# Performance work log

Measured on AMD Instinct MI355X. Metric: run time of the kernel, lower is better.

## Reference

```python
import jax, jax.numpy as jnp
import numpy as np

NUM_HEADS = 32
HEAD_DIM = 128
ROPE_THETA = 10000.0


def _rope_tables(seq_len, head_dim, theta):
    inv_freq = 1.0 / (theta ** (jnp.arange(0, head_dim, 2, dtype=jnp.float32) / head_dim))
    pos = jnp.arange(seq_len, dtype=jnp.float32)
    freqs = pos[:, None] * inv_freq[None, :]            # [S, hd/2]
    emb = jnp.concatenate([freqs, freqs], axis=-1)      # [S, hd]
    return jnp.cos(emb), jnp.sin(emb)


def _rotate_half(x):
    x1, x2 = jnp.split(x, 2, axis=-1)
    return jnp.concatenate([-x2, x1], axis=-1)


def _apply_rope(x, cos, sin):
    # x: [B, S, H, D]; cos/sin: [S, D] -> unsqueeze_dim=2 broadcasting
    c = cos[None, :, None, :]
    s = sin[None, :, None, :]
    return x * c + _rotate_half(x) * s


def setup_inputs() -> dict:
    key = jax.random.key(0)
    ks = jax.random.split(key, 6)
    hidden = 4096
    B, S = 2, 4096  # global sequence = world_size * local_seq (4 * 1024)
    hidden_states = jax.random.normal(ks[0], (B, S, hidden), dtype=jnp.float32)
    # original uses torch.rand (uniform); scaled by 0.02 for numerical sanity
    q_proj = jax.random.uniform(ks[1], (hidden, hidden), dtype=jnp.float32) * 0.02
    k_proj = jax.random.uniform(ks[2], (hidden, hidden), dtype=jnp.float32) * 0.02
    v_proj = jax.random.uniform(ks[3], (hidden, hidden), dtype=jnp.float32) * 0.02
    o_proj = jax.random.uniform(ks[4], (hidden, hidden), dtype=jnp.float32) * 0.02
    return {"hidden_states": hidden_states, "q_proj": q_proj, "k_proj": k_proj,
            "v_proj": v_proj, "o_proj": o_proj, "world_size": 4}


def _ring_attention(hidden_states, q_proj, k_proj, v_proj, o_proj, world_size):
    B, S, H = hidden_states.shape
    s_local = S // world_size
    nh, hd = NUM_HEADS, HEAD_DIM
    scale = 1.0 / np.sqrt(hd).astype(np.float32)

    # rank 0 holds the first sequence shard as its local hidden states
    hs_local = hidden_states[:, :s_local]
    q = (hs_local @ q_proj.T).reshape(B, s_local, nh, hd)
    k = (hidden_states @ k_proj.T).reshape(B, S, nh, hd)
    v = (hidden_states @ v_proj.T).reshape(B, S, nh, hd)

    cos, sin = _rope_tables(S, hd, ROPE_THETA)
    q = _apply_rope(q, cos[:s_local], sin[:s_local])   # rank0 positions 0..s_local-1
    k = _apply_rope(k, cos, sin)                       # global positions per shard

    # split into per-rank KV blocks; rank 0 receives blocks W-1, W-2, ..., 0
    k_blocks = k.reshape(B, world_size, s_local, nh, hd).transpose(1, 0, 2, 3, 4)[::-1]
    v_blocks = v.reshape(B, world_size, s_local, nh, hd).transpose(1, 0, 2, 3, 4)[::-1]

    def step(carry, kv):
        attn, max_lse, denom, lse_full = carry
        k_blk, v_blk = kv
        # memory_efficient_attention_partial: non-causal partial attention + lse
        s = jnp.einsum('bqhd,bkhd->bhqk', q, k_blk) * scale
        m = jnp.max(s, axis=-1)                          # [B,H,q]
        p = jnp.exp(s - m[..., None])
        l = jnp.sum(p, axis=-1)
        lse = (m + jnp.log(l)).transpose(0, 2, 1)        # [B,q,H]
        out = jnp.einsum('bhqk,bkhd->bqhd', p / l[..., None], v_blk)
        # online-softmax merge across ring steps
        new_max = jnp.maximum(max_lse, lse)
        old_adj = jnp.exp(max_lse - new_max)[..., None]
        new_adj = jnp.exp(lse - new_max)[..., None]
        denom = old_adj * denom + new_adj
        attn = old_adj * attn + new_adj * out
        lse_full = new_max + jnp.log(jnp.exp(lse_full - new_max) + jnp.exp(lse - new_max))
        return (attn, new_max, denom, lse_full), None

    init = (jnp.zeros((B, s_local, nh, hd), jnp.float32),
            jnp.full((B, s_local, nh), -jnp.inf, jnp.float32),
            jnp.zeros((B, s_local, nh, 1), jnp.float32),
            jnp.full((B, s_local, nh), -jnp.inf, jnp.float32))
    (attn, _, denom, _), _ = jax.lax.scan(step, init, (k_blocks, v_blocks))

    attn = attn / denom
    attn = attn.astype(jnp.float16).astype(jnp.float32)  # .half() in source
    attn = attn.reshape(B, s_local, nh * hd)
    return attn @ o_proj.T


def reference(hidden_states, q_proj, k_proj, v_proj, o_proj, world_size):
    return _ring_attention(hidden_states, q_proj, k_proj, v_proj, o_proj, world_size)
```

## Files before the change

kernel.cpp:

```cpp
#include <hip/hip_runtime.h>
#include <hip/hip_bf16.h>


using bf16x8 = __attribute__((ext_vector_type(8))) short;
using f32x4  = __attribute__((ext_vector_type(4))) float;

__device__ inline unsigned short f32_to_bf16_bits(float f) {
  unsigned int u = __float_as_uint(f);
  u += 0x7FFFu + ((u >> 16) & 1u);
  return (unsigned short)(u >> 16);
}
__device__ inline float bf16_bits_to_f32(unsigned short h) {
  return __uint_as_float(((unsigned int)h) << 16);
}
__device__ inline unsigned short f32_to_bf16_fast(float f) {
  __hip_bfloat16 hb = __float2bfloat16(f);
  unsigned short us;
  __builtin_memcpy(&us, &hb, 2);
  return us;
}

__device__ __forceinline__ void load_lds16(const unsigned short* g, unsigned short* l) {
  __builtin_amdgcn_global_load_lds(
      (const __attribute__((address_space(1))) void*)g,
      (__attribute__((address_space(3))) void*)l, 16, 0, 0);
}

__global__ void cast_f32_bf16_batched(const float* __restrict__ hs,
                                      const float* __restrict__ w0,
                                      const float* __restrict__ w1,
                                      const float* __restrict__ w2,
                                      const float* __restrict__ w3,
                                      unsigned short* __restrict__ out) {
  const long hs4 = 2L * 4096 * 4096 / 4;
  const long w4  = 4096L * 4096 / 4;
  long i = (long)blockIdx.x * blockDim.x + threadIdx.x;
  long stride = (long)gridDim.x * blockDim.x;
  const long total = hs4 + 4 * w4;
  for (; i < total; i += stride) {
    const float* src;
    long j = i;
    if (j < hs4) { src = hs; }
    else {
      j -= hs4;
      long wi = j / w4;
      j -= wi * w4;
      src = (wi == 0) ? w0 : (wi == 1) ? w1 : (wi == 2) ? w2 : w3;
    }
    float4 v = reinterpret_cast<const float4*>(src)[j];
    ushort4 o;
    o.x = f32_to_bf16_bits(v.x);
    o.y = f32_to_bf16_bits(v.y);
    o.z = f32_to_bf16_bits(v.z);
    o.w = f32_to_bf16_bits(v.w);
    reinterpret_cast<ushort4*>(out)[i] = o;
  }
}

__global__ void rope_tables(float* __restrict__ cos_t, float* __restrict__ sin_t) {
  int idx = blockIdx.x * 256 + threadIdx.x;
  if (idx >= 4096 * 64) return;
  int p = idx >> 6, i = idx & 63;
  float inv = __expf(-(float)i * (9.210340371976184f / 64.0f));
  float f = (float)p * inv;
  cos_t[idx] = cosf(f);
  sin_t[idx] = sinf(f);
}

__global__ void rope_apply_qk(unsigned short* __restrict__ qbuf,
                              unsigned short* __restrict__ kbuf,
                              const float4* __restrict__ cos4,
                              const float4* __restrict__ sin4,
                              float qgain) {
  const long qch = 2048L * 256;
  const long kch = 8192L * 256;
  long idx = (long)blockIdx.x * 256 + threadIdx.x;
  if (idx >= qch + kch) return;
  unsigned short* buf;
  int pos_mask; float gain;
  if (idx < qch) { buf = qbuf; pos_mask = 1023; gain = qgain; }
  else { idx -= qch; buf = kbuf; pos_mask = 4095; gain = 1.0f; }
  long tok = idx >> 8;
  int rem = (int)(idx & 255);
  int head = rem >> 3, c = rem & 7;
  int pos = (int)(tok & (long)pos_mask);
  float4 ct0 = cos4[pos * 16 + c * 2];
  float4 ct1 = cos4[pos * 16 + c * 2 + 1];
  float4 st0 = sin4[pos * 16 + c * 2];
  float4 st1 = sin4[pos * 16 + c * 2 + 1];
  float cs[8] = {ct0.x, ct0.y, ct0.z, ct0.w, ct1.x, ct1.y, ct1.z, ct1.w};
  float sn[8] = {st0.x, st0.y, st0.z, st0.w, st1.x, st1.y, st1.z, st1.w};
  long base = tok * 4096 + head * 128 + c * 8;
  bf16x8 x1 = *reinterpret_cast<const bf16x8*>(buf + base);
  bf16x8 x2 = *reinterpret_cast<const bf16x8*>(buf + base + 64);
  bf16x8 o1, o2;
#pragma unroll
  for (int j = 0; j < 8; j++) {
    float a = bf16_bits_to_f32((unsigned short)x1[j]);
    float b = bf16_bits_to_f32((unsigned short)x2[j]);
    o1[j] = (short)f32_to_bf16_bits((a * cs[j] - b * sn[j]) * gain);
    o2[j] = (short)f32_to_bf16_bits((b * cs[j] + a * sn[j]) * gain);
  }
  *reinterpret_cast<bf16x8*>(buf + base) = o1;
  *reinterpret_cast<bf16x8*>(buf + base + 64) = o2;
}

__device__ inline void storeC(float* p, float v) { *p = v; }
__device__ inline void storeC(unsigned short* p, float v) { *p = f32_to_bf16_bits(v); }

#define STG2(Gb, Lb, h, kc)                                                    \
  load_lds16((Gb) + (long)((h) * 128 + srow) * 4096 + sslot * 8 + (kc),        \
             (Lb) + tid * 8);                                                  \
  load_lds16((Gb) + (long)((h) * 128 + 64 + srow) * 4096 + sslot * 8 + (kc),   \
             (Lb) + 4096 + tid * 8);

#define MFMAQ(MH, NH)                                                          \
  _Pragma("unroll") for (int mi = 0; mi < 4; ++mi)                             \
    _Pragma("unroll") for (int ni = 0; ni < 2; ++ni)                           \
      _Pragma("unroll") for (int kk = 0; kk < 2; ++kk)                         \
        acc[(MH) * 4 + mi][(NH) * 2 + ni] =                                    \
            __builtin_amdgcn_mfma_f32_16x16x32_bf16(                           \
                a[mi][kk], b[(NH) * 2 + ni][kk],                               \
                acc[(MH) * 4 + mi][(NH) * 2 + ni], 0, 0, 0);

#define TILE(P, KC, MODE)                                                      \
  {                                                                            \
    const unsigned short* Ar = lds + wm * 16384 + (P) * 8192;                  \
    const unsigned short* Br =                                                 \
        lds + 32768 + (wn >> 1) * 16384 + (P) * 8192 + (wn & 1) * 4096;        \
    _Pragma("unroll") for (int mf = 0; mf < 4; ++mf) {                         \
      a[mf][0] = *reinterpret_cast<const bf16x8*>(Ar + mf * 1024 + ao0);       \
      a[mf][1] = *reinterpret_cast<const bf16x8*>(Ar + mf * 1024 + ao1);       \
    }                                                                          \
    _Pragma("unroll") for (int nf = 0; nf < 2; ++nf) {                         \
      b[nf][0] = *reinterpret_cast<const bf16x8*>(Br + nf * 1024 + ao0);       \
      b[nf][1] = *reinterpret_cast<const bf16x8*>(Br + nf * 1024 + ao1);       \
    }                                                                          \
    __builtin_amdgcn_s_setprio(1);                                             \
    MFMAQ(0, 0);                                                               \
    __builtin_amdgcn_s_setprio(0);                                             \
    _Pragma("unroll") for (int nf = 2; nf < 4; ++nf) {                         \
      b[nf][0] = *reinterpret_cast<const bf16x8*>(Br + nf * 1024 + ao0);       \
      b[nf][1] = *reinterpret_cast<const bf16x8*>(Br + nf * 1024 + ao1);       \
    }                                                                          \
    __builtin_amdgcn_s_setprio(1);                                             \
    MFMAQ(0, 1);                                                               \
    __builtin_amdgcn_s_setprio(0);                                             \
    asm volatile("s_waitcnt lgkmcnt(0)" ::: "memory");                         \
    asm volatile("s_barrier" ::: "memory");            \
    if ((MODE) == 0) {                                                         \
      STG2(Bg, lds + 32768 + (P) * 8192, 0, KC);                               \
      STG2(Bg, lds + 49152 + (P) * 8192, 1, KC);                               \
    }                                                                          \
    _Pragma("unroll") for (int mf = 0; mf < 4; ++mf) {                         \
      a[mf][0] = *reinterpret_cast<const bf16x8*>(Ar + (4 + mf) * 1024 + ao0); \
      a[mf][1] = *reinterpret_cast<const bf16x8*>(Ar + (4 + mf) * 1024 + ao1); \
    }                                                                          \
    __builtin_amdgcn_s_setprio(1);                                             \
    MFMAQ(1, 0);                                                               \
    __builtin_amdgcn_s_setprio(0);                                             \
    asm volatile("s_waitcnt lgkmcnt(0)" ::: "memory");                         \
    asm volatile("s_barrier" ::: "memory");            \
    if ((MODE) == 0) {                                                         \
      STG2(Ag, lds + (P) * 8192, 0, KC);                                       \
      STG2(Ag, lds + 16384 + (P) * 8192, 1, KC);                               \
    }                                                                          \
    __builtin_amdgcn_s_setprio(1);                                             \
    MFMAQ(1, 1);                                                               \
    __builtin_amdgcn_s_setprio(0);                                             \
    if ((MODE) == 0) asm volatile("s_waitcnt vmcnt(8)" ::: "memory");          \
    if ((MODE) == 1) asm volatile("s_waitcnt vmcnt(0)" ::: "memory");          \
    asm volatile("s_barrier" ::: "memory");       \
  }

template <typename OUT_T>
__global__ __launch_bounds__(512, 2) void gemm256(const unsigned short* __restrict__ A,
                                                  const unsigned short* __restrict__ B,
                                                  OUT_T* __restrict__ C,
                                                  long Astride_z, long Cstride_z, int N) {
  __shared__ unsigned short lds[65536];
  const int tid = threadIdx.x;
  const int bn = blockIdx.x, bm = blockIdx.y, bz = blockIdx.z;
  const unsigned short* Ag = A + (long)bz * Astride_z + (long)bm * 256 * 4096;
  const unsigned short* Bg = B + (long)bn * 256 * 4096;

  const int w = tid >> 6, lane = tid & 63;
  const int wm = w >> 2, wn = w & 3;
  const int fr = lane & 15, fg = lane >> 4;
  const int ao0 = fr * 64 + ((fg ^ (fr & 7)) * 8);
  const int ao1 = fr * 64 + (((4 + fg) ^ (fr & 7)) * 8);
  const int srow = tid >> 3;
  const int sslot = (tid & 7) ^ (srow & 7);

  f32x4 acc[8][4] = {};
  bf16x8 a[4][2], b[4][2];

  STG2(Ag, lds + 0, 0, 0);     STG2(Ag, lds + 16384, 1, 0);
  STG2(Bg, lds + 32768, 0, 0); STG2(Bg, lds + 49152, 1, 0);
  STG2(Ag, lds + 8192, 0, 64);  STG2(Ag, lds + 24576, 1, 64);
  STG2(Bg, lds + 40960, 0, 64); STG2(Bg, lds + 57344, 1, 64);
  asm volatile("s_waitcnt vmcnt(8)" ::: "memory");
  asm volatile("s_barrier" ::: "memory");

  for (int ti = 0; ti < 31; ++ti) {
    TILE(0, (2 * ti + 2) * 64, 0);
    TILE(1, (2 * ti + 3) * 64, 0);
  }
  TILE(0, 0, 1);
  TILE(1, 0, 2);

  OUT_T* Cb = C + (long)bz * Cstride_z + ((long)bm * 256) * N + bn * 256;
#pragma unroll
  for (int mf = 0; mf < 8; ++mf)
#pragma unroll
    for (int nf = 0; nf < 4; ++nf)
#pragma unroll
      for (int rr = 0; rr < 4; ++rr) {
        int row = wm * 128 + mf * 16 + fg * 4 + rr;
        int col = wn * 64 + nf * 16 + fr;
        storeC(Cb + (long)row * N + col, acc[mf][nf][rr]);
      }
}

__global__ __launch_bounds__(256) void attn_fwd(const unsigned short* __restrict__ qb,
                                                const unsigned short* __restrict__ kb,
                                                const unsigned short* __restrict__ vT,
                                                unsigned short* __restrict__ ob) {
  __shared__ unsigned short Ks[2][64 * 128];
  __shared__ unsigned short Vl[2][128 * 64];
  __shared__ unsigned short Ps[4][16 * 72];

  const int id = blockIdx.x;
  const int xcd = id & 7, j = id >> 3;
  const int hb = xcd + 8 * (j >> 4);
  const int qt = j & 15;
  const int h = hb & 31, b = hb >> 5;

  const int tid = threadIdx.x, w = tid >> 6, lane = tid & 63;
  const int fr = lane & 15, fg = lane >> 4;

  const unsigned short* kbase = kb + (long)b * 4096 * 4096 + h * 128;
  const unsigned short* vbase = vT + (long)h * 128 * 8192 + (long)b * 4096;

  const unsigned short* kp[4];
  const unsigned short* vp[4];
  unsigned short* kl[4];
  unsigned short* vl[4];
#pragma unroll
  for (int i = 0; i < 4; i++) {
    int c = tid + 256 * i;
    int key = c >> 4, s0 = c & 15;
    kp[i] = kbase + (long)(64 + key) * 4096 + (s0 ^ (key & 15)) * 8;
    kl[i] = (unsigned short*)&Ks[0][c * 8];
    int f0 = c >> 3, s1 = c & 7;
    vp[i] = vbase + (long)f0 * 8192 + 64 + (s1 ^ (f0 & 7)) * 8;
    vl[i] = (unsigned short*)&Vl[0][c * 8];
  }
  const int pelem = 64 * 128;

  bf16x8 qf[4];
  {
    const unsigned short* qptr =
        qb + ((long)b * 1024 + qt * 64 + w * 16 + fr) * 4096 + h * 128 + fg * 8;
#pragma unroll
    for (int c = 0; c < 4; c++) qf[c] = *reinterpret_cast<const bf16x8*>(qptr + c * 32);
  }

  f32x4 outa[8] = {};
  float m_run[4], l_run[4];
#pragma unroll
  for (int r = 0; r < 4; r++) { m_run[r] = -1e30f; l_run[r] = 0.0f; }

#pragma unroll
  for (int i = 0; i < 4; i++) {
    int c = tid + 256 * i;
    int key = c >> 4, s0 = c & 15;
    load_lds16(kbase + (long)key * 4096 + (s0 ^ (key & 15)) * 8, &Ks[0][c * 8]);
    int f0 = c >> 3, s1 = c & 7;
    load_lds16(vbase + (long)f0 * 8192 + (s1 ^ (f0 & 7)) * 8, &Vl[0][c * 8]);
  }
  asm volatile("s_waitcnt vmcnt(0)" ::: "memory");
  asm volatile("s_barrier" ::: "memory");

  for (int t = 0; t < 64; ++t) {
    const int cur = t & 1;
    if (t < 63) {
      const int po = (cur ^ 1) * pelem;
#pragma unroll
      for (int i = 0; i < 4; i++) {
        load_lds16(kp[i], kl[i] + po);
        kp[i] += 64 * 4096;
        load_lds16(vp[i], vl[i] + po);
        vp[i] += 64;
      }
    }

    f32x4 sacc[4];
    __builtin_amdgcn_s_setprio(1);
#pragma unroll
    for (int ks = 0; ks < 4; ks++) {
      f32x4 aq = {0.f, 0.f, 0.f, 0.f};
#pragma unroll
      for (int cc = 0; cc < 4; cc++) {
        bf16x8 kf = *reinterpret_cast<const bf16x8*>(
            &Ks[cur][(ks * 16 + fr) * 128 + (((cc * 4 + fg) ^ fr) & 15) * 8]);
        aq = __builtin_amdgcn_mfma_f32_16x16x32_bf16(qf[cc], kf, aq, 0, 0, 0);
      }
      sacc[ks] = aq;
    }
    __builtin_amdgcn_s_setprio(0);

    float mxl[4];
    int need = 0;
#pragma unroll
    for (int r = 0; r < 4; r++) {
      mxl[r] = fmaxf(fmaxf(sacc[0][r], sacc[1][r]), fmaxf(sacc[2][r], sacc[3][r]));
      need |= (mxl[r] > m_run[r] + 11.5f) ? 1 : 0;
    }
    if (__any(need)) {
#pragma unroll
      for (int r = 0; r < 4; r++) {
        float mx = mxl[r];
        mx = fmaxf(mx, __shfl_xor(mx, 1));
        mx = fmaxf(mx, __shfl_xor(mx, 2));
        mx = fmaxf(mx, __shfl_xor(mx, 4));
        mx = fmaxf(mx, __shfl_xor(mx, 8));
        float mnew = fmaxf(m_run[r], mx);
        float ef = exp2f(m_run[r] - mnew);
        l_run[r] *= ef;
        m_run[r] = mnew;
#pragma unroll
        for (int ds = 0; ds < 8; ds++) outa[ds][r] *= ef;
      }
    }
#pragma unroll
    for (int r = 0; r < 4; r++) {
      float sum = 0.f;
#pragma unroll
      for (int ks = 0; ks < 4; ks++) {
        float pv = exp2f(sacc[ks][r] - m_run[r]);
        Ps[w][(fg * 4 + r) * 72 + ks * 16 + fr] = f32_to_bf16_fast(pv);
        sum += pv;
      }
      l_run[r] += sum;
    }

    __builtin_amdgcn_s_setprio(1);
#pragma unroll
    for (int c2 = 0; c2 < 2; c2++) {
      bf16x8 pf = *reinterpret_cast<const bf16x8*>(&Ps[w][fr * 72 + c2 * 32 + fg * 8]);
#pragma unroll
      for (int ds = 0; ds < 8; ds++) {
        int feat = ds * 16 + fr;
        int pch = ((c2 * 4 + fg) ^ (feat & 7)) & 7;
        bf16x8 vf = *reinterpret_cast<const bf16x8*>(&Vl[cur][feat * 64 + pch * 8]);
        outa[ds] = __builtin_amdgcn_mfma_f32_16x16x32_bf16(pf, vf, outa[ds], 0, 0, 0);
      }
    }
    __builtin_amdgcn_s_setprio(0);

    if (t < 63) {
      asm volatile("s_waitcnt vmcnt(0) lgkmcnt(0)" ::: "memory");
      asm volatile("s_barrier" ::: "memory");
    }
  }

#pragma unroll
  for (int r = 0; r < 4; r++) {
    float l = l_run[r];
    l += __shfl_xor(l, 1);
    l += __shfl_xor(l, 2);
    l += __shfl_xor(l, 4);
    l += __shfl_xor(l, 8);
    float inv = 1.0f / l;
    unsigned short* op =
        ob + ((long)b * 1024 + qt * 64 + w * 16 + fg * 4 + r) * 4096 + h * 128;
#pragma unroll
    for (int ds = 0; ds < 8; ds++) op[ds * 16 + fr] = f32_to_bf16_bits(outa[ds][r] * inv);
  }
}

extern "C" void kernel_launch(void* const* d_in, const int* in_sizes, int n_in,
                              void* d_out, int out_size, void* d_ws, size_t ws_size,
                              hipStream_t stream) {
  const float* hs = (const float*)d_in[0];
  const float* wq = (const float*)d_in[1];
  const float* wk = (const float*)d_in[2];
  const float* wv = (const float*)d_in[3];
  const float* wo = (const float*)d_in[4];
  float* out = (float*)d_out;

  const long hsN = 2L * 4096 * 4096;
  const long wN  = 4096L * 4096;

  unsigned short* hs_b = (unsigned short*)d_ws;
  unsigned short* wq_b = hs_b + hsN;
  unsigned short* wk_b = wq_b + wN;
  unsigned short* wv_b = wk_b + wN;
  unsigned short* wo_b = wv_b + wN;
  unsigned short* q_b  = wo_b + wN;
  unsigned short* k_b  = q_b + 2048L * 4096;
  unsigned short* vT_b = k_b + 8192L * 4096;
  unsigned short* at_b = vT_b + 8192L * 4096;
  float* cos_t = (float*)(at_b + 2048L * 4096);
  float* sin_t = cos_t + 4096 * 64;

  cast_f32_bf16_batched<<<dim3(8192), dim3(256), 0, stream>>>(
      hs, wq, wk, wv, wo, hs_b);

  rope_tables<<<dim3(1024), dim3(256), 0, stream>>>(cos_t, sin_t);

  gemm256<unsigned short><<<dim3(16, 4, 2), dim3(512), 0, stream>>>(
      hs_b, wq_b, q_b, 4096L * 4096, 1024L * 4096, 4096);
  gemm256<unsigned short><<<dim3(16, 16, 2), dim3(512), 0, stream>>>(
      hs_b, wk_b, k_b, 4096L * 4096, 4096L * 4096, 4096);
  gemm256<unsigned short><<<dim3(32, 16, 1), dim3(512), 0, stream>>>(
      wv_b, hs_b, vT_b, 0L, 0L, 8192);

  const float qgain = 0.08838834764831845f * 1.4426950408889634f;
  rope_apply_qk<<<dim3(10240), dim3(256), 0, stream>>>(
      q_b, k_b, (const float4*)cos_t, (const float4*)sin_t, qgain);

  attn_fwd<<<dim3(1024), dim3(256), 0, stream>>>(q_b, k_b, vT_b, at_b);

  gemm256<float><<<dim3(16, 8, 1), dim3(512), 0, stream>>>(
      at_b, wo_b, out, 0L, 0L, 4096);
}
```

Measured before the change: 1.011 ms.

## Fuse RoPE rotation into Q/K projection GEMM epilogue

Removes the separate rope_apply_qk pass. The Q and K GEMMs now apply the rotary embedding and Q scaling in their epilogue. Each warp's B-tile columns are remapped so that it holds both halves (d and d+64) of a head's 32-dim slice in registers. This avoids a full read-modify-write of the Q and K buffers and one kernel launch. The cost is extra cos/sin table loads in the epilogue and an extra template variant.

```diff
diff --git a/kernel.cpp b/kernel.cpp
--- a/kernel.cpp
+++ b/kernel.cpp
@@ -67,44 +67,6 @@
   sin_t[idx] = sinf(f);
 }
 
-__global__ void rope_apply_qk(unsigned short* __restrict__ qbuf,
-                              unsigned short* __restrict__ kbuf,
-                              const float4* __restrict__ cos4,
-                              const float4* __restrict__ sin4,
-                              float qgain) {
-  const long qch = 2048L * 256;
-  const long kch = 8192L * 256;
-  long idx = (long)blockIdx.x * 256 + threadIdx.x;
-  if (idx >= qch + kch) return;
-  unsigned short* buf;
-  int pos_mask; float gain;
-  if (idx < qch) { buf = qbuf; pos_mask = 1023; gain = qgain; }
-  else { idx -= qch; buf = kbuf; pos_mask = 4095; gain = 1.0f; }
-  long tok = idx >> 8;
-  int rem = (int)(idx & 255);
-  int head = rem >> 3, c = rem & 7;
-  int pos = (int)(tok & (long)pos_mask);
-  float4 ct0 = cos4[pos * 16 + c * 2];
-  float4 ct1 = cos4[pos * 16 + c * 2 + 1];
-  float4 st0 = sin4[pos * 16 + c * 2];
-  float4 st1 = sin4[pos * 16 + c * 2 + 1];
-  float cs[8] = {ct0.x, ct0.y, ct0.z, ct0.w, ct1.x, ct1.y, ct1.z, ct1.w};
-  float sn[8] = {st0.x, st0.y, st0.z, st0.w, st1.x, st1.y, st1.z, st1.w};
-  long base = tok * 4096 + head * 128 + c * 8;
-  bf16x8 x1 = *reinterpret_cast<const bf16x8*>(buf + base);
-  bf16x8 x2 = *reinterpret_cast<const bf16x8*>(buf + base + 64);
-  bf16x8 o1, o2;
-#pragma unroll
-  for (int j = 0; j < 8; j++) {
-    float a = bf16_bits_to_f32((unsigned short)x1[j]);
-    float b = bf16_bits_to_f32((unsigned short)x2[j]);
-    o1[j] = (short)f32_to_bf16_bits((a * cs[j] - b * sn[j]) * gain);
-    o2[j] = (short)f32_to_bf16_bits((b * cs[j] + a * sn[j]) * gain);
-  }
-  *reinterpret_cast<bf16x8*>(buf + base) = o1;
-  *reinterpret_cast<bf16x8*>(buf + base + 64) = o2;
-}
-
 __device__ inline void storeC(float* p, float v) { *p = v; }
 __device__ inline void storeC(unsigned short* p, float v) { *p = f32_to_bf16_bits(v); }
 
@@ -126,22 +88,21 @@
 #define TILE(P, KC, MODE)                                                      \
   {                                                                            \
     const unsigned short* Ar = lds + wm * 16384 + (P) * 8192;                  \
-    const unsigned short* Br =                                                 \
-        lds + 32768 + (wn >> 1) * 16384 + (P) * 8192 + (wn & 1) * 4096;        \
+    const unsigned short* Br = brw + (P) * 8192;                               \
     _Pragma("unroll") for (int mf = 0; mf < 4; ++mf) {                         \
       a[mf][0] = *reinterpret_cast<const bf16x8*>(Ar + mf * 1024 + ao0);       \
       a[mf][1] = *reinterpret_cast<const bf16x8*>(Ar + mf * 1024 + ao1);       \
     }                                                                          \
     _Pragma("unroll") for (int nf = 0; nf < 2; ++nf) {                         \
-      b[nf][0] = *reinterpret_cast<const bf16x8*>(Br + nf * 1024 + ao0);       \
-      b[nf][1] = *reinterpret_cast<const bf16x8*>(Br + nf * 1024 + ao1);       \
+      b[nf][0] = *reinterpret_cast<const bf16x8*>(Br + boff[nf] + ao0);        \
+      b[nf][1] = *reinterpret_cast<const bf16x8*>(Br + boff[nf] + ao1);        \
     }                                                                          \
     __builtin_amdgcn_s_setprio(1);                                             \
     MFMAQ(0, 0);                                                               \
     __builtin_amdgcn_s_setprio(0);                                             \
     _Pragma("unroll") for (int nf = 2; nf < 4; ++nf) {                         \
-      b[nf][0] = *reinterpret_cast<const bf16x8*>(Br + nf * 1024 + ao0);       \
-      b[nf][1] = *reinterpret_cast<const bf16x8*>(Br + nf * 1024 + ao1);       \
+      b[nf][0] = *reinterpret_cast<const bf16x8*>(Br + boff[nf] + ao0);        \
+      b[nf][1] = *reinterpret_cast<const bf16x8*>(Br + boff[nf] + ao1);        \
     }                                                                          \
     __builtin_amdgcn_s_setprio(1);                                             \
     MFMAQ(0, 1);                                                               \
@@ -173,11 +134,14 @@
     asm volatile("s_barrier" ::: "memory");       \
   }
 
-template <typename OUT_T>
+template <typename OUT_T, bool ROPE>
 __global__ __launch_bounds__(512, 2) void gemm256(const unsigned short* __restrict__ A,
                                                   const unsigned short* __restrict__ B,
                                                   OUT_T* __restrict__ C,
-                                                  long Astride_z, long Cstride_z, int N) {
+                                                  long Astride_z, long Cstride_z, int N,
+                                                  const float* __restrict__ cos_t,
+                                                  const float* __restrict__ sin_t,
+                                                  float gain) {
   __shared__ unsigned short lds[65536];
   const int tid = threadIdx.x;
   const int bn = blockIdx.x, bm = blockIdx.y, bz = blockIdx.z;
@@ -192,6 +156,13 @@
   const int srow = tid >> 3;
   const int sslot = (tid & 7) ^ (srow & 7);
 
+  const unsigned short* brw =
+      lds + 32768 + (wn >> 1) * 16384 + (ROPE ? (wn & 1) * 2048 : (wn & 1) * 4096);
+  int boff[4];
+#pragma unroll
+  for (int nf = 0; nf < 4; ++nf)
+    boff[nf] = ROPE ? ((nf & 1) * 1024 + (nf >> 1) * 4096) : nf * 1024;
+
   f32x4 acc[8][4] = {};
   bf16x8 a[4][2], b[4][2];
 
@@ -210,16 +181,36 @@
   TILE(1, 0, 2);
 
   OUT_T* Cb = C + (long)bz * Cstride_z + ((long)bm * 256) * N + bn * 256;
-#pragma unroll
-  for (int mf = 0; mf < 8; ++mf)
-#pragma unroll
-    for (int nf = 0; nf < 4; ++nf)
-#pragma unroll
-      for (int rr = 0; rr < 4; ++rr) {
-        int row = wm * 128 + mf * 16 + fg * 4 + rr;
-        int col = wn * 64 + nf * 16 + fr;
-        storeC(Cb + (long)row * N + col, acc[mf][nf][rr]);
-      }
+  if constexpr (ROPE) {
+    const int head = wn >> 1, q = wn & 1;
+#pragma unroll
+    for (int mf = 0; mf < 8; ++mf)
+#pragma unroll
+      for (int nf = 0; nf < 2; ++nf)
+#pragma unroll
+        for (int rr = 0; rr < 4; ++rr) {
+          int row = wm * 128 + mf * 16 + fg * 4 + rr;
+          int pos = bm * 256 + row;
+          int d = q * 32 + nf * 16 + fr;
+          float c = cos_t[pos * 64 + d];
+          float s = sin_t[pos * 64 + d];
+          float x1 = acc[mf][nf][rr];
+          float x2 = acc[mf][nf + 2][rr];
+          storeC(Cb + (long)row * N + head * 128 + d, (x1 * c - x2 * s) * gain);
+          storeC(Cb + (long)row * N + head * 128 + 64 + d, (x2 * c + x1 * s) * gain);
+        }
+  } else {
+#pragma unroll
+    for (int mf = 0; mf < 8; ++mf)
+#pragma unroll
+      for (int nf = 0; nf < 4; ++nf)
+#pragma unroll
+        for (int rr = 0; rr < 4; ++rr) {
+          int row = wm * 128 + mf * 16 + fg * 4 + rr;
+          int col = wn * 64 + nf * 16 + fr;
+          storeC(Cb + (long)row * N + col, acc[mf][nf][rr]);
+        }
+  }
 }
 
 __global__ __launch_bounds__(256) void attn_fwd(const unsigned short* __restrict__ qb,
@@ -410,19 +401,16 @@
 
   rope_tables<<<dim3(1024), dim3(256), 0, stream>>>(cos_t, sin_t);
 
-  gemm256<unsigned short><<<dim3(16, 4, 2), dim3(512), 0, stream>>>(
-      hs_b, wq_b, q_b, 4096L * 4096, 1024L * 4096, 4096);
-  gemm256<unsigned short><<<dim3(16, 16, 2), dim3(512), 0, stream>>>(
-      hs_b, wk_b, k_b, 4096L * 4096, 4096L * 4096, 4096);
-  gemm256<unsigned short><<<dim3(32, 16, 1), dim3(512), 0, stream>>>(
-      wv_b, hs_b, vT_b, 0L, 0L, 8192);
-
   const float qgain = 0.08838834764831845f * 1.4426950408889634f;
-  rope_apply_qk<<<dim3(10240), dim3(256), 0, stream>>>(
-      q_b, k_b, (const float4*)cos_t, (const float4*)sin_t, qgain);
+  gemm256<unsigned short, true><<<dim3(16, 4, 2), dim3(512), 0, stream>>>(
+      hs_b, wq_b, q_b, 4096L * 4096, 1024L * 4096, 4096, cos_t, sin_t, qgain);
+  gemm256<unsigned short, true><<<dim3(16, 16, 2), dim3(512), 0, stream>>>(
+      hs_b, wk_b, k_b, 4096L * 4096, 4096L * 4096, 4096, cos_t, sin_t, 1.0f);
+  gemm256<unsigned short, false><<<dim3(32, 16, 1), dim3(512), 0, stream>>>(
+      wv_b, hs_b, vT_b, 0L, 0L, 8192, cos_t, sin_t, 1.0f);
 
   attn_fwd<<<dim3(1024), dim3(256), 0, stream>>>(q_b, k_b, vT_b, at_b);
 
-  gemm256<float><<<dim3(16, 8, 1), dim3(512), 0, stream>>>(
-      at_b, wo_b, out, 0L, 0L, 4096);
-}
+  gemm256<float, false><<<dim3(16, 8, 1), dim3(512), 0, stream>>>(
+      at_b, wo_b, out, 0L, 0L, 4096, cos_t, sin_t, 1.0f);
+}
```

After: 1.006 ms. Within noise of the previous version (-0.5%).
